# Performance work log

Hardware: AMD Instinct MI355X
Metric: run time of the kernel (lower is better)

## Reference

```python
import jax, jax.numpy as jnp
import numpy as np

N = 50000      # nodes
E = 800000     # edges (before self loops)
D_IN = 256
D_H = 256
D_OUT = 64     # num_classes
SLOPE = 0.01   # leaky_relu slope


def setup_inputs() -> dict:
    key = jax.random.key(0)
    ks = jax.random.split(key, 8)
    x = jax.random.normal(ks[0], (N, D_IN), dtype=jnp.float32)
    edge_index = jax.random.randint(ks[1], (2, E), 0, N, dtype=jnp.int32)
    s = 0.05
    W1 = jax.random.normal(ks[2], (D_H, D_IN), dtype=jnp.float32) * s
    b1 = jnp.zeros((D_H,), dtype=jnp.float32)
    W2 = jax.random.normal(ks[3], (D_H, D_H), dtype=jnp.float32) * s
    b2 = jnp.zeros((D_H,), dtype=jnp.float32)
    W3 = jax.random.normal(ks[4], (D_OUT, D_H), dtype=jnp.float32) * s
    b3 = jnp.zeros((D_OUT,), dtype=jnp.float32)
    return {"x": x, "edge_index": edge_index, "W1": W1, "b1": b1,
            "W2": W2, "b2": b2, "W3": W3, "b3": b3}


def _gcn_layer(x, W, b, src, dst):
    # PyG GCNConv: h = x @ W^T; out[dst] += d^{-1/2}[src] d^{-1/2}[dst] * h[src]; out += b
    h = x @ W.T                                             # [N, out]
    ones = jnp.ones(src.shape[0], dtype=h.dtype)
    deg = jax.ops.segment_sum(ones, dst, num_segments=N)    # includes self loops
    dinv = jnp.where(deg > 0, jax.lax.rsqrt(deg), 0.0)
    norm = dinv[src] * dinv[dst]                            # [E+N]
    msg = h[src] * norm[:, None]                            # gather + scale
    out = jax.ops.segment_sum(msg, dst, num_segments=N)     # scatter-add
    return out + b


def reference(x, edge_index, W1, b1, W2, b2, W3, b3):
    src, dst = edge_index[0], edge_index[1]
    loop = jnp.arange(N, dtype=src.dtype)                   # add self loops
    src = jnp.concatenate([src, loop])
    dst = jnp.concatenate([dst, loop])
    act = lambda h: jax.nn.leaky_relu(h, negative_slope=SLOPE)
    h1 = act(_gcn_layer(x, W1, b1, src, dst))
    h2 = act(_gcn_layer(h1, W2, b2, src, dst))
    logits = _gcn_layer(h2, W3, b3, src, dst)               # no activation on last layer
    return (h1, h2, logits)
```

## Files before the change

### kernel.cpp

```cpp
#include <hip/hip_runtime.h>

#define N_NODES 50000
#define E_EDGES 800000
#define SLOPE 0.01f

typedef __attribute__((ext_vector_type(8))) short bf16x8;
typedef __attribute__((ext_vector_type(4))) float floatx4;
typedef __attribute__((ext_vector_type(4))) float f32x4;
typedef __attribute__((ext_vector_type(2))) float f32x2;
typedef __attribute__((ext_vector_type(2))) unsigned int u32x2;

__device__ __forceinline__ unsigned short f2bf(float f) {
    unsigned u = __builtin_bit_cast(unsigned, f);
    unsigned r = (u + 0x7FFFu + ((u >> 16) & 1u)) >> 16;
    return (unsigned short)r;
}
__device__ __forceinline__ float bf2f(unsigned short h) {
    unsigned u = ((unsigned)h) << 16;
    return __builtin_bit_cast(float, u);
}
__device__ __forceinline__ float blo(unsigned u) { return __builtin_bit_cast(float, u << 16); }
__device__ __forceinline__ float bhi(unsigned u) { return __builtin_bit_cast(float, u & 0xFFFF0000u); }
__device__ __forceinline__ f32x2 up2(unsigned u) {
    f32x2 t; t.x = blo(u); t.y = bhi(u); return t;
}

__device__ __forceinline__ void acc8p(uint4 v, f32x2 a[4]) {
    a[0] += up2(v.x); a[1] += up2(v.y); a[2] += up2(v.z); a[3] += up2(v.w);
}
__device__ __forceinline__ void acc4p(uint2 v, f32x2 a[2]) {
    a[0] += up2(v.x); a[1] += up2(v.y);
}


__device__ __forceinline__ void conv_body(const float* __restrict__ in,
                                          unsigned short* __restrict__ out, int i, int n4) {
    if (i < n4) {
        float4 v = ((const float4*)in)[i];
        ushort4 o;
        o.x = f2bf(v.x); o.y = f2bf(v.y); o.z = f2bf(v.z); o.w = f2bf(v.w);
        ((ushort4*)out)[i] = o;
    }
}

__device__ __forceinline__ void wfrag_body(const float* __restrict__ Wf,
                                           unsigned short* __restrict__ out, int idx, int n4) {
    if (idx >= n4) return;
    int n = idx >> 6;
    int k = (idx & 63) << 2;
    float4 v = ((const float4*)Wf)[idx];
    int jt = n >> 4, lm = n & 15, kk = k >> 5, q = (k >> 3) & 3, e = k & 7;
    int off = ((jt * 8 + kk) * 64 + q * 16 + lm) * 8 + e;
    ushort4 o;
    o.x = f2bf(v.x); o.y = f2bf(v.y); o.z = f2bf(v.z); o.w = f2bf(v.w);
    *(ushort4*)(out + off) = o;
}

#define PREP_HIST_B   3125
#define PREP_CONV_B   12500
#define PREP_W1_B     64
#define PREP_W2_B     64
#define PREP_W3_B     16
#define PREP_TOTAL_B  (PREP_HIST_B + PREP_CONV_B + PREP_W1_B + PREP_W2_B + PREP_W3_B)

__global__ __launch_bounds__(256) void prep0_kernel(
        const float* __restrict__ x, unsigned short* __restrict__ xb,
        const float* __restrict__ W1, unsigned short* __restrict__ W1f,
        const float* __restrict__ W2, unsigned short* __restrict__ W2f,
        const float* __restrict__ W3, unsigned short* __restrict__ W3f,
        const int* __restrict__ dst, int* __restrict__ counts,
        unsigned short* __restrict__ rank) {
    int b = blockIdx.x, tid = threadIdx.x;
    if (b < PREP_HIST_B) {
        int e = b * 256 + tid;
        if (e < E_EDGES) {
            int d = dst[e];
            rank[e] = (unsigned short)atomicAdd(&counts[d], 1);
        }
    } else if (b < PREP_HIST_B + PREP_CONV_B) {
        conv_body(x, xb, (b - PREP_HIST_B) * 256 + tid, N_NODES * 256 / 4);
    } else if (b < PREP_HIST_B + PREP_CONV_B + PREP_W1_B) {
        wfrag_body(W1, W1f, (b - PREP_HIST_B - PREP_CONV_B) * 256 + tid, 16384);
    } else if (b < PREP_HIST_B + PREP_CONV_B + PREP_W1_B + PREP_W2_B) {
        wfrag_body(W2, W2f, (b - PREP_HIST_B - PREP_CONV_B - PREP_W1_B) * 256 + tid, 16384);
    } else {
        wfrag_body(W3, W3f, (b - PREP_HIST_B - PREP_CONV_B - PREP_W1_B - PREP_W2_B) * 256 + tid, 4096);
    }
}


#define SB 1024
__global__ __launch_bounds__(SB) void scan1_dinv_kernel(const int* __restrict__ counts,
                                                        int* __restrict__ partial,
                                                        int* __restrict__ bsum,
                                                        float* __restrict__ dinv) {
    __shared__ int wsum[16];
    int tid = threadIdx.x, lane = tid & 63, wid = tid >> 6;
    int i = blockIdx.x * SB + tid;
    int v = (i < N_NODES) ? counts[i] : 0;
    int x = v;
    #pragma unroll
    for (int off = 1; off < 64; off <<= 1) {
        int y = __shfl_up(x, off, 64);
        if (lane >= off) x += y;
    }
    if (lane == 63) wsum[wid] = x;
    __syncthreads();
    if (wid == 0) {
        int s = (lane < 16) ? wsum[lane] : 0;
        #pragma unroll
        for (int off = 1; off < 16; off <<= 1) {
            int y = __shfl_up(s, off, 64);
            if (lane >= off) s += y;
        }
        if (lane < 16) wsum[lane] = s;
    }
    __syncthreads();
    int woff = wid ? wsum[wid - 1] : 0;
    if (i < N_NODES) {
        partial[i] = woff + x - v;
        dinv[i] = rsqrtf((float)(v + 1));
    }
    if (tid == SB - 1) bsum[blockIdx.x] = woff + x;
}

__global__ __launch_bounds__(256) void scan3b_kernel(int* __restrict__ row_ptr,
                                                     const int* __restrict__ bsum,
                                                     int nb) {
    __shared__ int pref[64];
    int tid = threadIdx.x;
    if (tid < 64) {
        int v = (tid < nb) ? bsum[tid] : 0;
        #pragma unroll
        for (int off = 1; off < 64; off <<= 1) {
            int y = __shfl_up(v, off, 64);
            if (tid >= off) v += y;
        }
        pref[tid] = v;
    }
    __syncthreads();
    int i = blockIdx.x * 256 + tid;
    if (i < N_NODES) {
        int c = i >> 10;
        int off = c ? pref[c - 1] : 0;
        row_ptr[i] += off;
    }
    if (i == 0) row_ptr[N_NODES] = pref[nb - 1];
}


template<int WAVES_M, int WAVES_N, int MT, int NT>
__device__ __forceinline__ void gemm_frag_body(
        int bx, int by, int tid,
        const unsigned short* __restrict__ Ab,
        const unsigned short* __restrict__ Bf,
        const float* __restrict__ dinv,
        unsigned short* __restrict__ C, int M, int Nc) {
    const int wave = tid >> 6, lane = tid & 63;
    const int lm = lane & 15, q = lane >> 4;
    const int bm = bx * (WAVES_M * MT * 16);
    const int bn = by * (WAVES_N * NT * 16);
    const int wm = (wave / WAVES_N) * (MT * 16);
    const int wn = (wave % WAVES_N) * (NT * 16);
    const int jt0 = (bn + wn) >> 4;

    const unsigned short* arow[MT];
    #pragma unroll
    for (int i = 0; i < MT; ++i) {
        int r = bm + wm + i * 16 + lm;
        if (r >= M) r = M - 1;
        arow[i] = Ab + (size_t)r * 256 + q * 8;
    }

    floatx4 acc[MT][NT] = {};

    #pragma unroll
    for (int kk = 0; kk < 8; ++kk) {
        bf16x8 a[MT], b[NT];
        #pragma unroll
        for (int i = 0; i < MT; ++i)
            a[i] = *(const bf16x8*)(arow[i] + kk * 32);
        #pragma unroll
        for (int j = 0; j < NT; ++j)
            b[j] = *(const bf16x8*)(Bf + (((jt0 + j) * 8 + kk) * 64 + lane) * 8);
        #pragma unroll
        for (int i = 0; i < MT; ++i)
            #pragma unroll
            for (int j = 0; j < NT; ++j)
                acc[i][j] = __builtin_amdgcn_mfma_f32_16x16x32_bf16(a[i], b[j], acc[i][j], 0, 0, 0);
    }

    #pragma unroll
    for (int i = 0; i < MT; ++i) {
        int rb = bm + wm + i * 16 + q * 4;
        #pragma unroll
        for (int r = 0; r < 4; ++r) {
            int row = rb + r;
            if (row < M) {
                float dd = dinv[row];
                #pragma unroll
                for (int j = 0; j < NT; ++j)
                    C[(size_t)row * Nc + bn + wn + j * 16 + lm] = f2bf(acc[i][j][r] * dd);
            }
        }
    }
}

__global__ __launch_bounds__(256) void gemm256_kernel(
        const unsigned short* __restrict__ Ab, const unsigned short* __restrict__ Bf,
        const float* __restrict__ dinv, unsigned short* __restrict__ C, int M, int Nc) {
    gemm_frag_body<2, 2, 4, 4>(blockIdx.x, blockIdx.y, threadIdx.x, Ab, Bf, dinv, C, M, Nc);
}

__global__ __launch_bounds__(256) void gemm64_kernel(
        const unsigned short* __restrict__ Ab, const unsigned short* __restrict__ Bf,
        const float* __restrict__ dinv, unsigned short* __restrict__ C, int M, int Nc) {
    gemm_frag_body<4, 1, 4, 4>(blockIdx.x, 0, threadIdx.x, Ab, Bf, dinv, C, M, Nc);
}

#define GEMM1_B 782
__global__ __launch_bounds__(256) void gemm1_place_kernel(
        const unsigned short* __restrict__ Ab, const unsigned short* __restrict__ Bf,
        const float* __restrict__ dinv, unsigned short* __restrict__ C, int M, int Nc,
        const int* __restrict__ src, const int* __restrict__ dst,
        const int* __restrict__ row_ptr, const unsigned short* __restrict__ rank,
        int* __restrict__ col_idx) {
    int b = blockIdx.x;
    if (b < PREP_HIST_B) {
        int e = b * 256 + threadIdx.x;
        if (e < E_EDGES) {
            int d = dst[e];
            col_idx[row_ptr[d] + (int)rank[e]] = src[e];
        }
    } else {
        int b2 = b - PREP_HIST_B;
        gemm_frag_body<2, 2, 4, 4>(b2 >> 1, b2 & 1, threadIdx.x, Ab, Bf, dinv, C, M, Nc);
    }
}


template<bool ACT>
__global__ __launch_bounds__(256) void agg256_kernel(
        const int* __restrict__ row_ptr, const int* __restrict__ col_idx,
        const float* __restrict__ dinv, const unsigned short* __restrict__ hs,
        const float* __restrict__ bias,
        float* __restrict__ out, unsigned short* __restrict__ outb) {
    int node = __builtin_amdgcn_readfirstlane(blockIdx.x * 4 + (threadIdx.x >> 6));
    int lane = threadIdx.x & 63;
    int half = lane >> 5, sl = lane & 31;

    f32x2 a[4] = {};

    int beg = row_ptr[node], end = row_ptr[node + 1];
    for (int cbeg = beg; cbeg < end; cbeg += 64) {
        int clen = end - cbeg; if (clen > 64) clen = 64;
        int cidx = (lane < clen) ? col_idx[cbeg + lane] : 0;

        int jj = 0;
        for (; jj + 8 <= clen; jj += 8) {
            int s0 = __shfl(cidx, jj + half);
            int s1 = __shfl(cidx, jj + 2 + half);
            int s2 = __shfl(cidx, jj + 4 + half);
            int s3 = __shfl(cidx, jj + 6 + half);
            uint4 v0 = ((const uint4*)(hs + (size_t)s0 * 256))[sl];
            uint4 v1 = ((const uint4*)(hs + (size_t)s1 * 256))[sl];
            uint4 v2 = ((const uint4*)(hs + (size_t)s2 * 256))[sl];
            uint4 v3 = ((const uint4*)(hs + (size_t)s3 * 256))[sl];
            acc8p(v0, a); acc8p(v1, a); acc8p(v2, a); acc8p(v3, a);
        }
        for (; jj + 2 <= clen; jj += 2) {
            int s = __shfl(cidx, jj + half);
            uint4 v = ((const uint4*)(hs + (size_t)s * 256))[sl];
            acc8p(v, a);
        }
        if (jj < clen) {
            int s = __shfl(cidx, jj);
            if (half == 0) {
                uint4 v = ((const uint4*)(hs + (size_t)s * 256))[sl];
                acc8p(v, a);
            }
        }
    }

    float s0 = a[0].x, s1 = a[0].y, s2 = a[1].x, s3 = a[1].y;
    float s4 = a[2].x, s5 = a[2].y, s6 = a[3].x, s7 = a[3].y;

    s0 += __shfl_xor(s0, 32); s1 += __shfl_xor(s1, 32);
    s2 += __shfl_xor(s2, 32); s3 += __shfl_xor(s3, 32);
    s4 += __shfl_xor(s4, 32); s5 += __shfl_xor(s5, 32);
    s6 += __shfl_xor(s6, 32); s7 += __shfl_xor(s7, 32);

    uint4 sv = ((const uint4*)(hs + (size_t)node * 256))[sl];
    s0 += blo(sv.x); s1 += bhi(sv.x);
    s2 += blo(sv.y); s3 += bhi(sv.y);
    s4 += blo(sv.z); s5 += bhi(sv.z);
    s6 += blo(sv.w); s7 += bhi(sv.w);

    int srcl = lane >> 1;
    float t0 = __shfl(s0, srcl), t1 = __shfl(s1, srcl);
    float t2 = __shfl(s2, srcl), t3 = __shfl(s3, srcl);
    float t4 = __shfl(s4, srcl), t5 = __shfl(s5, srcl);
    float t6 = __shfl(s6, srcl), t7 = __shfl(s7, srcl);
    bool hi = (lane & 1);
    float f0 = hi ? t4 : t0, f1 = hi ? t5 : t1, f2 = hi ? t6 : t2, f3 = hi ? t7 : t3;

    float dd = dinv[node];
    const float4 b4 = ((const float4*)bias)[lane];
    f0 = fmaf(f0, dd, b4.x); f1 = fmaf(f1, dd, b4.y);
    f2 = fmaf(f2, dd, b4.z); f3 = fmaf(f3, dd, b4.w);
    if (ACT) {
        f0 = f0 > 0.f ? f0 : SLOPE * f0;
        f1 = f1 > 0.f ? f1 : SLOPE * f1;
        f2 = f2 > 0.f ? f2 : SLOPE * f2;
        f3 = f3 > 0.f ? f3 : SLOPE * f3;
    }
    f32x4 o = {f0, f1, f2, f3};
    __builtin_nontemporal_store(o, (f32x4*)(out + (size_t)node * 256) + lane);
    u32x2 obv;
    obv.x = ((unsigned)f2bf(f1) << 16) | f2bf(f0);
    obv.y = ((unsigned)f2bf(f3) << 16) | f2bf(f2);
    ((u32x2*)(outb + (size_t)node * 256))[lane] = obv;
}

__global__ __launch_bounds__(256) void agg64_kernel(
        const int* __restrict__ row_ptr, const int* __restrict__ col_idx,
        const float* __restrict__ dinv, const unsigned short* __restrict__ hs,
        const float* __restrict__ bias, float* __restrict__ out) {
    int node = __builtin_amdgcn_readfirstlane(blockIdx.x * 4 + (threadIdx.x >> 6));
    int lane = threadIdx.x & 63;
    int g = lane >> 4, sl = lane & 15;

    f32x2 a[2] = {};

    int beg = row_ptr[node], end = row_ptr[node + 1];
    for (int cbeg = beg; cbeg < end; cbeg += 64) {
        int clen = end - cbeg; if (clen > 64) clen = 64;
        int cidx = (lane < clen) ? col_idx[cbeg + lane] : 0;

        int jj = 0;
        for (; jj + 8 <= clen; jj += 8) {
            int s0 = __shfl(cidx, jj + g);
            int s1 = __shfl(cidx, jj + 4 + g);
            uint2 v0 = ((const uint2*)(hs + (size_t)s0 * 64))[sl];
            uint2 v1 = ((const uint2*)(hs + (size_t)s1 * 64))[sl];
            acc4p(v0, a); acc4p(v1, a);
        }
        for (; jj + 4 <= clen; jj += 4) {
            int s = __shfl(cidx, jj + g);
            uint2 v = ((const uint2*)(hs + (size_t)s * 64))[sl];
            acc4p(v, a);
        }
        int rem = clen - jj;
        if (rem > 0) {
            int s = __shfl(cidx, jj + g);
            if (g < rem) {
                uint2 v = ((const uint2*)(hs + (size_t)s * 64))[sl];
                acc4p(v, a);
            }
        }
    }

    float s0 = a[0].x, s1 = a[0].y, s2 = a[1].x, s3 = a[1].y;

    s0 += __shfl_xor(s0, 16); s0 += __shfl_xor(s0, 32);
    s1 += __shfl_xor(s1, 16); s1 += __shfl_xor(s1, 32);
    s2 += __shfl_xor(s2, 16); s2 += __shfl_xor(s2, 32);
    s3 += __shfl_xor(s3, 16); s3 += __shfl_xor(s3, 32);

    uint2 sv = ((const uint2*)(hs + (size_t)node * 64))[sl];
    s0 += blo(sv.x); s1 += bhi(sv.x);
    s2 += blo(sv.y); s3 += bhi(sv.y);

    float dd = dinv[node];
    const float4 b4 = ((const float4*)bias)[sl];
    f32x4 o;
    o[0] = fmaf(s0, dd, b4.x);
    o[1] = fmaf(s1, dd, b4.y);
    o[2] = fmaf(s2, dd, b4.z);
    o[3] = fmaf(s3, dd, b4.w);
    if (g == 0)
        __builtin_nontemporal_store(o, (f32x4*)(out + (size_t)node * 64) + sl);
}


static inline int cdiv(long long a, long long b) { return (int)((a + b - 1) / b); }

extern "C" void kernel_launch(void* const* d_in, const int* in_sizes, int n_in,
                              void* d_out, int out_size, void* d_ws, size_t ws_size,
                              hipStream_t stream) {
    const float* x  = (const float*)d_in[0];
    const int* ei   = (const int*)d_in[1];
    const float* W1 = (const float*)d_in[2];
    const float* b1 = (const float*)d_in[3];
    const float* W2 = (const float*)d_in[4];
    const float* b2 = (const float*)d_in[5];
    const float* W3 = (const float*)d_in[6];
    const float* b3 = (const float*)d_in[7];

    const int* src = ei;
    const int* dst = ei + E_EDGES;

    char* ws = (char*)d_ws;
    int*   row_ptr = (int*)ws;   ws += 50112 * 4;
    float* dinv    = (float*)ws; ws += 50048 * 4;
    int*   bsum    = (int*)ws;   ws += 64 * 4;
    unsigned short* rank = (unsigned short*)ws; ws += (size_t)E_EDGES * 2;
    int*   col_idx = (int*)ws;   ws += (size_t)E_EDGES * 4;
    unsigned short* W1f = (unsigned short*)ws; ws += 65536 * 2;
    unsigned short* W2f = (unsigned short*)ws; ws += 65536 * 2;
    unsigned short* W3f = (unsigned short*)ws; ws += 16384 * 2;
    unsigned short* hb  = (unsigned short*)ws; ws += (size_t)N_NODES * 256 * 2;
    unsigned short* ob  = (unsigned short*)ws;

    int* counts = (int*)hb;

    float* out1 = (float*)d_out;
    float* out2 = out1 + (size_t)N_NODES * 256;
    float* out3 = out2 + (size_t)N_NODES * 256;

    const int NB = cdiv(N_NODES, SB);

    (void)hipMemsetAsync(counts, 0, 50048 * sizeof(int), stream);
    prep0_kernel<<<PREP_TOTAL_B, 256, 0, stream>>>(x, ob, W1, W1f, W2, W2f, W3, W3f,
                                                   dst, counts, rank);

    scan1_dinv_kernel<<<NB, SB, 0, stream>>>(counts, row_ptr, bsum, dinv);
    scan3b_kernel<<<cdiv(N_NODES, 256), 256, 0, stream>>>(row_ptr, bsum, NB);

    dim3 g256(cdiv(N_NODES, 128), 2);
    int agg_grid = cdiv(N_NODES, 4);

    gemm1_place_kernel<<<PREP_HIST_B + GEMM1_B, 256, 0, stream>>>(
        ob, W1f, dinv, hb, N_NODES, 256, src, dst, row_ptr, rank, col_idx);
    agg256_kernel<true><<<agg_grid, 256, 0, stream>>>(row_ptr, col_idx, dinv, hb, b1, out1, ob);

    gemm256_kernel<<<g256, 256, 0, stream>>>(ob, W2f, dinv, hb, N_NODES, 256);
    agg256_kernel<true><<<agg_grid, 256, 0, stream>>>(row_ptr, col_idx, dinv, hb, b2, out2, ob);

    gemm64_kernel<<<cdiv(N_NODES, 256), 256, 0, stream>>>(ob, W3f, dinv, hb, N_NODES, 64);
    agg64_kernel<<<agg_grid, 256, 0, stream>>>(row_ptr, col_idx, dinv, hb, b3, out3);
}
```

Baseline: 421.4 us.

## Slice hidden features into 64-column planes and aggregate per slice

```diff
diff --git a/kernel.cpp b/kernel.cpp
--- a/kernel.cpp
+++ b/kernel.cpp
@@ -3,12 +3,14 @@
 #define N_NODES 50000
 #define E_EDGES 800000
 #define SLOPE 0.01f
+#define SS ((size_t)N_NODES * 64)
 
 typedef __attribute__((ext_vector_type(8))) short bf16x8;
 typedef __attribute__((ext_vector_type(4))) float floatx4;
 typedef __attribute__((ext_vector_type(4))) float f32x4;
 typedef __attribute__((ext_vector_type(2))) float f32x2;
 typedef __attribute__((ext_vector_type(2))) unsigned int u32x2;
+typedef __attribute__((ext_vector_type(4))) unsigned int u32x4;
 
 __device__ __forceinline__ unsigned short f2bf(float f) {
     unsigned u = __builtin_bit_cast(unsigned, f);
@@ -149,7 +151,7 @@
 }
 
 
-template<int WAVES_M, int WAVES_N, int MT, int NT>
+template<int WAVES_M, int WAVES_N, int MT, int NT, bool SLICED>
 __device__ __forceinline__ void gemm_frag_body(
         int bx, int by, int tid,
         const unsigned short* __restrict__ Ab,
@@ -199,8 +201,13 @@
             if (row < M) {
                 float dd = dinv[row];
                 #pragma unroll
-                for (int j = 0; j < NT; ++j)
-                    C[(size_t)row * Nc + bn + wn + j * 16 + lm] = f2bf(acc[i][j][r] * dd);
+                for (int j = 0; j < NT; ++j) {
+                    int col = bn + wn + j * 16 + lm;
+                    size_t addr = SLICED
+                        ? ((size_t)(col >> 6) * SS + (size_t)row * 64 + (col & 63))
+                        : ((size_t)row * Nc + col);
+                    C[addr] = f2bf(acc[i][j][r] * dd);
+                }
             }
         }
     }
@@ -209,13 +216,13 @@
 __global__ __launch_bounds__(256) void gemm256_kernel(
         const unsigned short* __restrict__ Ab, const unsigned short* __restrict__ Bf,
         const float* __restrict__ dinv, unsigned short* __restrict__ C, int M, int Nc) {
-    gemm_frag_body<2, 2, 4, 4>(blockIdx.x, blockIdx.y, threadIdx.x, Ab, Bf, dinv, C, M, Nc);
+    gemm_frag_body<2, 2, 4, 4, true>(blockIdx.x, blockIdx.y, threadIdx.x, Ab, Bf, dinv, C, M, Nc);
 }
 
 __global__ __launch_bounds__(256) void gemm64_kernel(
         const unsigned short* __restrict__ Ab, const unsigned short* __restrict__ Bf,
         const float* __restrict__ dinv, unsigned short* __restrict__ C, int M, int Nc) {
-    gemm_frag_body<4, 1, 4, 4>(blockIdx.x, 0, threadIdx.x, Ab, Bf, dinv, C, M, Nc);
+    gemm_frag_body<4, 1, 4, 4, false>(blockIdx.x, 0, threadIdx.x, Ab, Bf, dinv, C, M, Nc);
 }
 
 #define GEMM1_B 782
@@ -234,7 +241,7 @@
         }
     } else {
         int b2 = b - PREP_HIST_B;
-        gemm_frag_body<2, 2, 4, 4>(b2 >> 1, b2 & 1, threadIdx.x, Ab, Bf, dinv, C, M, Nc);
+        gemm_frag_body<2, 2, 4, 4, true>(b2 >> 1, b2 & 1, threadIdx.x, Ab, Bf, dinv, C, M, Nc);
     }
 }
 
@@ -246,8 +253,10 @@
         const float* __restrict__ bias,
         float* __restrict__ out, unsigned short* __restrict__ outb) {
     int node = __builtin_amdgcn_readfirstlane(blockIdx.x * 4 + (threadIdx.x >> 6));
+    int slice = blockIdx.y;
+    const unsigned short* hsl = hs + (size_t)slice * SS;
     int lane = threadIdx.x & 63;
-    int half = lane >> 5, sl = lane & 31;
+    int g = lane >> 3, sl = lane & 7;
 
     f32x2 a[4] = {};
 
@@ -257,26 +266,23 @@
         int cidx = (lane < clen) ? col_idx[cbeg + lane] : 0;
 
         int jj = 0;
+        for (; jj + 16 <= clen; jj += 16) {
+            int s0 = __shfl(cidx, jj + g);
+            int s1 = __shfl(cidx, jj + 8 + g);
+            uint4 v0 = ((const uint4*)(hsl + (size_t)s0 * 64))[sl];
+            uint4 v1 = ((const uint4*)(hsl + (size_t)s1 * 64))[sl];
+            acc8p(v0, a); acc8p(v1, a);
+        }
         for (; jj + 8 <= clen; jj += 8) {
-            int s0 = __shfl(cidx, jj + half);
-            int s1 = __shfl(cidx, jj + 2 + half);
-            int s2 = __shfl(cidx, jj + 4 + half);
-            int s3 = __shfl(cidx, jj + 6 + half);
-            uint4 v0 = ((const uint4*)(hs + (size_t)s0 * 256))[sl];
-            uint4 v1 = ((const uint4*)(hs + (size_t)s1 * 256))[sl];
-            uint4 v2 = ((const uint4*)(hs + (size_t)s2 * 256))[sl];
-            uint4 v3 = ((const uint4*)(hs + (size_t)s3 * 256))[sl];
-            acc8p(v0, a); acc8p(v1, a); acc8p(v2, a); acc8p(v3, a);
-        }
-        for (; jj + 2 <= clen; jj += 2) {
-            int s = __shfl(cidx, jj + half);
-            uint4 v = ((const uint4*)(hs + (size_t)s * 256))[sl];
+            int s = __shfl(cidx, jj + g);
+            uint4 v = ((const uint4*)(hsl + (size_t)s * 64))[sl];
             acc8p(v, a);
         }
-        if (jj < clen) {
-            int s = __shfl(cidx, jj);
-            if (half == 0) {
-                uint4 v = ((const uint4*)(hs + (size_t)s * 256))[sl];
+        int rem = clen - jj;
+        if (rem > 0) {
+            int s = __shfl(cidx, jj + g);
+            if (g < rem) {
+                uint4 v = ((const uint4*)(hsl + (size_t)s * 64))[sl];
                 acc8p(v, a);
             }
         }
@@ -285,41 +291,46 @@
     float s0 = a[0].x, s1 = a[0].y, s2 = a[1].x, s3 = a[1].y;
     float s4 = a[2].x, s5 = a[2].y, s6 = a[3].x, s7 = a[3].y;
 
-    s0 += __shfl_xor(s0, 32); s1 += __shfl_xor(s1, 32);
-    s2 += __shfl_xor(s2, 32); s3 += __shfl_xor(s3, 32);
-    s4 += __shfl_xor(s4, 32); s5 += __shfl_xor(s5, 32);
-    s6 += __shfl_xor(s6, 32); s7 += __shfl_xor(s7, 32);
-
-    uint4 sv = ((const uint4*)(hs + (size_t)node * 256))[sl];
+    #pragma unroll
+    for (int m = 8; m <= 32; m <<= 1) {
+        s0 += __shfl_xor(s0, m); s1 += __shfl_xor(s1, m);
+        s2 += __shfl_xor(s2, m); s3 += __shfl_xor(s3, m);
+        s4 += __shfl_xor(s4, m); s5 += __shfl_xor(s5, m);
+        s6 += __shfl_xor(s6, m); s7 += __shfl_xor(s7, m);
+    }
+
+    uint4 sv = ((const uint4*)(hsl + (size_t)node * 64))[sl];
     s0 += blo(sv.x); s1 += bhi(sv.x);
     s2 += blo(sv.y); s3 += bhi(sv.y);
     s4 += blo(sv.z); s5 += bhi(sv.z);
     s6 += blo(sv.w); s7 += bhi(sv.w);
 
-    int srcl = lane >> 1;
-    float t0 = __shfl(s0, srcl), t1 = __shfl(s1, srcl);
-    float t2 = __shfl(s2, srcl), t3 = __shfl(s3, srcl);
-    float t4 = __shfl(s4, srcl), t5 = __shfl(s5, srcl);
-    float t6 = __shfl(s6, srcl), t7 = __shfl(s7, srcl);
-    bool hi = (lane & 1);
-    float f0 = hi ? t4 : t0, f1 = hi ? t5 : t1, f2 = hi ? t6 : t2, f3 = hi ? t7 : t3;
-
     float dd = dinv[node];
-    const float4 b4 = ((const float4*)bias)[lane];
-    f0 = fmaf(f0, dd, b4.x); f1 = fmaf(f1, dd, b4.y);
-    f2 = fmaf(f2, dd, b4.z); f3 = fmaf(f3, dd, b4.w);
+    const float4 b40 = ((const float4*)bias)[slice * 16 + sl * 2];
+    const float4 b41 = ((const float4*)bias)[slice * 16 + sl * 2 + 1];
+    float f0 = fmaf(s0, dd, b40.x), f1 = fmaf(s1, dd, b40.y);
+    float f2 = fmaf(s2, dd, b40.z), f3 = fmaf(s3, dd, b40.w);
+    float f4 = fmaf(s4, dd, b41.x), f5 = fmaf(s5, dd, b41.y);
+    float f6 = fmaf(s6, dd, b41.z), f7 = fmaf(s7, dd, b41.w);
     if (ACT) {
-        f0 = f0 > 0.f ? f0 : SLOPE * f0;
-        f1 = f1 > 0.f ? f1 : SLOPE * f1;
-        f2 = f2 > 0.f ? f2 : SLOPE * f2;
-        f3 = f3 > 0.f ? f3 : SLOPE * f3;
-    }
-    f32x4 o = {f0, f1, f2, f3};
-    __builtin_nontemporal_store(o, (f32x4*)(out + (size_t)node * 256) + lane);
-    u32x2 obv;
-    obv.x = ((unsigned)f2bf(f1) << 16) | f2bf(f0);
-    obv.y = ((unsigned)f2bf(f3) << 16) | f2bf(f2);
-    ((u32x2*)(outb + (size_t)node * 256))[lane] = obv;
+        f0 = f0 > 0.f ? f0 : SLOPE * f0;  f1 = f1 > 0.f ? f1 : SLOPE * f1;
+        f2 = f2 > 0.f ? f2 : SLOPE * f2;  f3 = f3 > 0.f ? f3 : SLOPE * f3;
+        f4 = f4 > 0.f ? f4 : SLOPE * f4;  f5 = f5 > 0.f ? f5 : SLOPE * f5;
+        f6 = f6 > 0.f ? f6 : SLOPE * f6;  f7 = f7 > 0.f ? f7 : SLOPE * f7;
+    }
+    if (g == 0) {
+        float* op = out + (size_t)node * 256 + slice * 64 + sl * 8;
+        f32x4 o0 = {f0, f1, f2, f3};
+        f32x4 o1 = {f4, f5, f6, f7};
+        __builtin_nontemporal_store(o0, (f32x4*)op);
+        __builtin_nontemporal_store(o1, (f32x4*)op + 1);
+        u32x4 ob;
+        ob.x = ((unsigned)f2bf(f1) << 16) | f2bf(f0);
+        ob.y = ((unsigned)f2bf(f3) << 16) | f2bf(f2);
+        ob.z = ((unsigned)f2bf(f5) << 16) | f2bf(f4);
+        ob.w = ((unsigned)f2bf(f7) << 16) | f2bf(f6);
+        *(u32x4*)(outb + (size_t)node * 256 + slice * 64 + sl * 8) = ob;
+    }
 }
 
 __global__ __launch_bounds__(256) void agg64_kernel(
@@ -428,15 +439,15 @@
     scan3b_kernel<<<cdiv(N_NODES, 256), 256, 0, stream>>>(row_ptr, bsum, NB);
 
     dim3 g256(cdiv(N_NODES, 128), 2);
-    int agg_grid = cdiv(N_NODES, 4);
+    dim3 agg_g(cdiv(N_NODES, 4), 4);
 
     gemm1_place_kernel<<<PREP_HIST_B + GEMM1_B, 256, 0, stream>>>(
         ob, W1f, dinv, hb, N_NODES, 256, src, dst, row_ptr, rank, col_idx);
-    agg256_kernel<true><<<agg_grid, 256, 0, stream>>>(row_ptr, col_idx, dinv, hb, b1, out1, ob);
+    agg256_kernel<true><<<agg_g, 256, 0, stream>>>(row_ptr, col_idx, dinv, hb, b1, out1, ob);
 
     gemm256_kernel<<<g256, 256, 0, stream>>>(ob, W2f, dinv, hb, N_NODES, 256);
-    agg256_kernel<true><<<agg_grid, 256, 0, stream>>>(row_ptr, col_idx, dinv, hb, b2, out2, ob);
+    agg256_kernel<true><<<agg_g, 256, 0, stream>>>(row_ptr, col_idx, dinv, hb, b2, out2, ob);
 
     gemm64_kernel<<<cdiv(N_NODES, 256), 256, 0, stream>>>(ob, W3f, dinv, hb, N_NODES, 64);
-    agg64_kernel<<<agg_grid, 256, 0, stream>>>(row_ptr, col_idx, dinv, hb, b3, out3);
-}
+    agg64_kernel<<<cdiv(N_NODES, 4), 256, 0, stream>>>(row_ptr, col_idx, dinv, hb, b3, out3);
+}
```

Result: slower. 450.7 us (+6.9%).
